# Kernel optimization log

Measured on AMD Instinct MI355X. Metric: run time of the kernel, lower is better.

Reference implementation:

```python
import math
import jax, jax.numpy as jnp
import numpy as np

B, T, C, H = 2, 2048, 1024, 16
MAX_SEQ = 2048


def _make_pe(max_seq: int, dim: int, base: float = 10000.0) -> np.ndarray:
    pe = np.zeros((max_seq, dim), dtype=np.float32)
    position = np.arange(max_seq, dtype=np.float32)[:, None]
    div_term = np.exp(np.arange(0, dim, 2, dtype=np.float32) * (-math.log(base) / dim))
    pe[:, 0::2] = np.sin(position * div_term)
    pe[:, 1::2] = np.cos(position * div_term)
    return pe


def setup_inputs() -> dict:
    key = jax.random.key(0)
    k1, k2, k3 = jax.random.split(key, 3)
    x = jax.random.normal(k1, (B, T, C), dtype=jnp.float32)
    # torch Linear default init scale ~ 1/sqrt(fan_in)
    w_qkv = jax.random.normal(k2, (3 * C, C), dtype=jnp.float32) / math.sqrt(C)
    w_proj = jax.random.normal(k3, (C, C), dtype=jnp.float32) / math.sqrt(C)
    pe = jnp.asarray(_make_pe(MAX_SEQ, C))
    return {"x": x, "w_qkv": w_qkv, "w_proj": w_proj, "pe": pe}


def reference(x, w_qkv, w_proj, pe):
    b, t, c = x.shape
    h = H
    d = c // h
    # RoPE module adds sinusoidal PE under torch.no_grad() -> stop_gradient
    xp = jax.lax.stop_gradient(x + pe[None, :t, :])
    qkv = xp @ w_qkv.T  # [b, t, 3c]
    q, k, v = jnp.split(qkv, 3, axis=-1)
    q = q.reshape(b, t, h, d).transpose(0, 2, 1, 3)  # bhtd
    k = k.reshape(b, t, h, d).transpose(0, 2, 1, 3)
    v = v.reshape(b, t, h, d).transpose(0, 2, 1, 3)
    att = jnp.einsum("bhqd,bhkd->bhqk", q, k) * (1.0 / math.sqrt(d))
    causal = jnp.tril(jnp.ones((t, t), dtype=bool))  # [t, t]
    att = jnp.where(causal[None, None], att, -jnp.inf)
    att = jax.nn.softmax(att, axis=-1)
    y = jnp.einsum("bhqk,bhkd->bhqd", att, v)
    y = y.transpose(0, 2, 1, 3).reshape(b, t, c)
    return y @ w_proj.T
```

## Files before the change

### kernel.cpp

```cpp
#include <hip/hip_runtime.h>
#include <cstdint>

typedef __bf16 bf16x8 __attribute__((ext_vector_type(8)));
typedef __bf16 bf16x4 __attribute__((ext_vector_type(4)));
typedef float  f32x4  __attribute__((ext_vector_type(4)));

static constexpr int kB = 2, kT = 2048, kC = 1024, kH = 16, kD = 64;
static constexpr int kK = 1024;

__device__ __forceinline__ uint16_t f2bf(float f) {
  uint32_t u = __builtin_bit_cast(uint32_t, f);
  u += 0x7FFFu + ((u >> 16) & 1u);
  return (uint16_t)(u >> 16);
}

__device__ __forceinline__ void gl_lds16(const void* g, void* l) {
  __builtin_amdgcn_global_load_lds((__attribute__((address_space(1))) void*)(void*)g,
                                   (__attribute__((address_space(3))) void*)l, 16, 0, 0);
}

__global__ __launch_bounds__(256) void prep_xpe(const float* __restrict__ x,
                                                const float* __restrict__ pe,
                                                uint16_t* __restrict__ xp) {
  const int i = blockIdx.x * 256 + threadIdx.x;
  const float4 xv = ((const float4*)x)[i];
  const int c4 = i & (kC / 4 - 1);
  const int t = (i / (kC / 4)) & (kT - 1);
  const float4 pv = ((const float4*)pe)[t * (kC / 4) + c4];
  ushort4 o;
  o.x = f2bf(xv.x + pv.x);
  o.y = f2bf(xv.y + pv.y);
  o.z = f2bf(xv.z + pv.z);
  o.w = f2bf(xv.w + pv.w);
  ((ushort4*)xp)[i] = o;
}

__global__ __launch_bounds__(256) void cast_w(const float* __restrict__ w,
                                              uint16_t* __restrict__ o) {
  const int i = blockIdx.x * 256 + threadIdx.x;
  const float4 v = ((const float4*)w)[i];
  ushort4 u;
  u.x = f2bf(v.x); u.y = f2bf(v.y); u.z = f2bf(v.z); u.w = f2bf(v.w);
  ((ushort4*)o)[i] = u;
}

template <int EPI>
__global__ __launch_bounds__(256) void gemm_bt(const uint16_t* __restrict__ A,
                                               const uint16_t* __restrict__ W,
                                               uint16_t* __restrict__ qb,
                                               uint16_t* __restrict__ kb,
                                               uint16_t* __restrict__ vT,
                                               float* __restrict__ out) {
  __shared__ __align__(1024) char lds[EPI == 0 ? 34816 : 32768];
  const int lane = threadIdx.x & 63;
  const int wid = threadIdx.x >> 6;
  const int l15 = lane & 15, l4 = lane >> 4;
  const int wm = wid >> 1, wn = wid & 1;
  const int orig = (int)(blockIdx.y * gridDim.x + blockIdx.x);
  const int xcd = orig & 7, j = orig >> 3;
  const int m0 = (xcd * 4 + (j & 3)) * 128;
  const int n0 = (j >> 2) * 128;

  f32x4 acc[4][4] = {};

  for (int k0 = 0; k0 < kK; k0 += 64) {
#pragma unroll
    for (int jj = 0; jj < 4; ++jj) {
      const int off = wid * 4096 + jj * 1024 + lane * 16;
      const int row = off >> 7;
      const int colb = (off & 127) ^ ((row & 7) << 4);
      gl_lds16((const char*)A + ((size_t)(m0 + row) * kK + k0) * 2 + colb,
               lds + wid * 4096 + jj * 1024);
      gl_lds16((const char*)W + ((size_t)(n0 + row) * kK + k0) * 2 + colb,
               lds + 16384 + wid * 4096 + jj * 1024);
    }
    __syncthreads();
#pragma unroll
    for (int ks = 0; ks < 2; ++ks) {
      bf16x8 af[4], bf_[4];
#pragma unroll
      for (int mt = 0; mt < 4; ++mt) {
        const int r = wm * 64 + mt * 16 + l15;
        const int cb = (l4 * 16 + ks * 64) ^ ((r & 7) << 4);
        af[mt] = *(const bf16x8*)(lds + r * 128 + cb);
      }
#pragma unroll
      for (int nt = 0; nt < 4; ++nt) {
        const int r = wn * 64 + nt * 16 + l15;
        const int cb = (l4 * 16 + ks * 64) ^ ((r & 7) << 4);
        bf_[nt] = *(const bf16x8*)(lds + 16384 + r * 128 + cb);
      }
#pragma unroll
      for (int mt = 0; mt < 4; ++mt)
#pragma unroll
        for (int nt = 0; nt < 4; ++nt)
          acc[mt][nt] = __builtin_amdgcn_mfma_f32_16x16x32_bf16(af[mt], bf_[nt],
                                                                acc[mt][nt], 0, 0, 0);
    }
    __syncthreads();
  }

  if constexpr (EPI == 0) {
    const int sec = n0 >> 10;
    if (sec < 2) {
#pragma unroll
      for (int mt = 0; mt < 4; ++mt)
#pragma unroll
        for (int nt = 0; nt < 4; ++nt)
#pragma unroll
          for (int r = 0; r < 4; ++r) {
            const int m = wm * 64 + mt * 16 + l4 * 4 + r;
            const int n = wn * 64 + nt * 16 + l15;
            *(uint16_t*)(lds + m * 272 + ((n * 2) ^ (((m >> 2) & 3) << 4))) =
                f2bf(acc[mt][nt][r]);
          }
    } else {
#pragma unroll
      for (int mt = 0; mt < 4; ++mt)
#pragma unroll
        for (int nt = 0; nt < 4; ++nt)
#pragma unroll
          for (int r = 0; r < 4; ++r) {
            const int m = wm * 64 + mt * 16 + l4 * 4 + r;
            const int n = wn * 64 + nt * 16 + l15;
            *(uint16_t*)(lds + n * 272 + m * 2) = f2bf(acc[mt][nt][r]);
          }
    }
    __syncthreads();
    const int tid = threadIdx.x;
    const int b = m0 >> 11, tbase = m0 & (kT - 1);
    if (sec < 2) {
      uint16_t* dst = (sec == 0) ? qb : kb;
#pragma unroll
      for (int i = 0; i < 8; ++i) {
        const int g = i * 256 + tid;
        const int ml = g >> 4;
        const int c8 = (g & 15) * 8;
        const bf16x8 v =
            *(const bf16x8*)(lds + ml * 272 + ((c8 * 2) ^ (((ml >> 2) & 3) << 4)));
        const int nn = (n0 & (kC - 1)) + c8;
        const int h = nn >> 6, d = nn & 63;
        *(bf16x8*)(dst + ((size_t)((b * kH + h) * kT + tbase + ml)) * kD + d) = v;
      }
    } else {
#pragma unroll
      for (int i = 0; i < 8; ++i) {
        const int g = i * 256 + tid;
        const int dl = g >> 4;
        const int m8 = (g & 15) * 8;
        const bf16x8 v = *(const bf16x8*)(lds + dl * 272 + m8 * 2);
        const int nn = (n0 & (kC - 1)) + dl;
        const int h = nn >> 6, d = nn & 63;
        *(bf16x8*)(vT + ((size_t)((b * kH + h) * kD + d)) * kT + tbase + m8) = v;
      }
    }
  } else {
#pragma unroll
    for (int mt = 0; mt < 4; ++mt)
#pragma unroll
      for (int nt = 0; nt < 4; ++nt)
#pragma unroll
        for (int r = 0; r < 4; ++r) {
          const int m = m0 + wm * 64 + mt * 16 + l4 * 4 + r;
          const int n = n0 + wn * 64 + nt * 16 + l15;
          out[(size_t)m * kC + n] = acc[mt][nt][r];
        }
  }
}

__global__ __launch_bounds__(256, 4) void attn(const uint16_t* __restrict__ qb,
                                               const uint16_t* __restrict__ kb,
                                               const uint16_t* __restrict__ vT,
                                               uint16_t* __restrict__ y) {
  __shared__ __align__(1024) char lds[40960];
  const int lane = threadIdx.x & 63;
  const int wid = threadIdx.x >> 6;
  const int l15 = lane & 15, l4 = lane >> 4;
  const int bh = blockIdx.x;
  const int qt = (int)(gridDim.y - 1) - (int)blockIdx.y;
  const int q0 = qt * 64 + wid * 16;
  const size_t base = (size_t)bh * kT * kD;
  const uint16_t* Q = qb + base;
  const uint16_t* Kp = kb + base;
  const uint16_t* Vt = vT + base;
  char* P = lds + 32768 + wid * 2048;
  const int xr = (l15 & 7) << 4;

  bf16x8 qf[2];
#pragma unroll
  for (int ks = 0; ks < 2; ++ks) {
    bf16x8 t = *(const bf16x8*)(Q + (size_t)(q0 + l15) * kD + ks * 32 + l4 * 8);
#pragma unroll
    for (int i = 0; i < 8; ++i) t[i] = (__bf16)((float)t[i] * 0.1803368801f);
    qf[ks] = t;
  }

  float m_ = -1e30f, l_ = 0.f;
  f32x4 o[4];
#pragma unroll
  for (int nt = 0; nt < 4; ++nt) o[nt] = (f32x4){0.f, 0.f, 0.f, 0.f};

  const int nkt = qt + 1;

  auto STAGE = [&](int bi, int k0) {
#pragma unroll
    for (int c = 0; c < 2; ++c) {
      const int call = wid * 2 + c;
      const int row = call * 8 + (lane >> 3);
      const int colb = (((lane & 7) ^ ((lane >> 3) & 7)) << 4);
      gl_lds16((const char*)Kp + ((size_t)(k0 + row) * kD) * 2 + colb,
               lds + bi * 8192 + call * 1024);
      gl_lds16((const char*)Vt + ((size_t)row * kT + k0) * 2 + colb,
               lds + 16384 + bi * 8192 + call * 1024);
    }
  };

  int cur = 0;
  STAGE(0, 0);
  for (int kt = 0; kt < nkt; ++kt) {
    const int k0 = kt * 64;
    const bool hasnext = (kt + 1 < nkt);
    if (hasnext) STAGE(cur ^ 1, k0 + 64);
    if (hasnext)
      asm volatile("s_waitcnt vmcnt(4)" ::: "memory");
    else
      asm volatile("s_waitcnt vmcnt(0)" ::: "memory");
    __builtin_amdgcn_s_barrier();
    asm volatile("" ::: "memory");

    const char* Kb = lds + cur * 8192;
    const char* Vb = lds + 16384 + cur * 8192;

    f32x4 s[4] = {};
    __builtin_amdgcn_s_setprio(1);
#pragma unroll
    for (int ks = 0; ks < 2; ++ks)
#pragma unroll
      for (int nt = 0; nt < 4; ++nt) {
        const bf16x8 kf =
            *(const bf16x8*)(Kb + (nt * 16 + l15) * 128 + ((ks * 64 + l4 * 16) ^ xr));
        s[nt] = __builtin_amdgcn_mfma_f32_16x16x32_bf16(kf, qf[ks], s[nt], 0, 0, 0);
      }
    __builtin_amdgcn_s_setprio(0);

    if (kt == nkt - 1) {
      const int qq = q0 + l15;
#pragma unroll
      for (int nt = 0; nt < 4; ++nt)
#pragma unroll
        for (int r = 0; r < 4; ++r)
          if (k0 + nt * 16 + l4 * 4 + r > qq) s[nt][r] = -1e30f;
    }

    float pm = s[0][0];
#pragma unroll
    for (int nt = 0; nt < 4; ++nt)
#pragma unroll
      for (int r = 0; r < 4; ++r) pm = fmaxf(pm, s[nt][r]);
    if (!__all(pm <= m_ + 11.0f)) {
      float rm = fmaxf(pm, __shfl_xor(pm, 16));
      rm = fmaxf(rm, __shfl_xor(rm, 32));
      const float newm = fmaxf(m_, rm);
      const float sc = exp2f(m_ - newm);
      m_ = newm;
      l_ *= sc;
#pragma unroll
      for (int nt = 0; nt < 4; ++nt)
#pragma unroll
        for (int r = 0; r < 4; ++r) o[nt][r] *= sc;
    }
    float ps = 0.f;
#pragma unroll
    for (int nt = 0; nt < 4; ++nt)
#pragma unroll
      for (int r = 0; r < 4; ++r) {
        const float p = exp2f(s[nt][r] - m_);
        s[nt][r] = p;
        ps += p;
      }
    l_ += ps;

#pragma unroll
    for (int nt = 0; nt < 4; ++nt) {
      bf16x4 pk;
#pragma unroll
      for (int r = 0; r < 4; ++r) pk[r] = (__bf16)s[nt][r];
      *(bf16x4*)(P + l15 * 128 + ((nt * 32 + l4 * 8) ^ xr)) = pk;
    }
    asm volatile("s_waitcnt lgkmcnt(0)" ::: "memory");
    __builtin_amdgcn_sched_barrier(0);

    bf16x8 pf[2];
#pragma unroll
    for (int ks = 0; ks < 2; ++ks)
      pf[ks] = *(const bf16x8*)(P + l15 * 128 + ((ks * 64 + l4 * 16) ^ xr));
    __builtin_amdgcn_s_setprio(1);
#pragma unroll
    for (int ks = 0; ks < 2; ++ks)
#pragma unroll
      for (int nt = 0; nt < 4; ++nt) {
        const bf16x8 vf =
            *(const bf16x8*)(Vb + (nt * 16 + l15) * 128 + ((ks * 64 + l4 * 16) ^ xr));
        o[nt] = __builtin_amdgcn_mfma_f32_16x16x32_bf16(vf, pf[ks], o[nt], 0, 0, 0);
      }
    __builtin_amdgcn_s_setprio(0);

    __builtin_amdgcn_s_barrier();
    asm volatile("" ::: "memory");
    cur ^= 1;
  }

  l_ += __shfl_xor(l_, 16);
  l_ += __shfl_xor(l_, 32);
  const float inv = 1.0f / l_;
  const int b = bh >> 4, h = bh & 15;
  const int q = q0 + l15;
#pragma unroll
  for (int nt = 0; nt < 4; ++nt) {
    bf16x4 yv;
#pragma unroll
    for (int r = 0; r < 4; ++r) yv[r] = (__bf16)(o[nt][r] * inv);
    *(bf16x4*)(y + ((size_t)(b * kT + q)) * kC + h * kD + nt * 16 + l4 * 4) = yv;
  }
}

extern "C" void kernel_launch(void* const* d_in, const int* in_sizes, int n_in,
                              void* d_out, int out_size, void* d_ws, size_t ws_size,
                              hipStream_t stream) {
  const float* x = (const float*)d_in[0];
  const float* wqkv = (const float*)d_in[1];
  const float* wproj = (const float*)d_in[2];
  const float* pe = (const float*)d_in[3];

  char* ws = (char*)d_ws;
  uint16_t* xp = (uint16_t*)(ws);
  uint16_t* wq = (uint16_t*)(ws + (size_t)(8u << 20));
  uint16_t* wp = (uint16_t*)(ws + (size_t)(14u << 20));
  uint16_t* qbuf = (uint16_t*)(ws + (size_t)(16u << 20));
  uint16_t* kbuf = (uint16_t*)(ws + (size_t)(24u << 20));
  uint16_t* vTb = (uint16_t*)(ws + (size_t)(32u << 20));

  prep_xpe<<<dim3(kB * kT * kC / 4 / 256), 256, 0, stream>>>(x, pe, xp);
  cast_w<<<dim3(3 * kC * kC / 4 / 256), 256, 0, stream>>>(wqkv, wq);
  cast_w<<<dim3(kC * kC / 4 / 256), 256, 0, stream>>>(wproj, wp);

  gemm_bt<0><<<dim3(32, 24), 256, 0, stream>>>(xp, wq, qbuf, kbuf, vTb, nullptr);

  attn<<<dim3(kB * kH, kT / 64), 256, 0, stream>>>(qbuf, kbuf, vTb, xp);

  gemm_bt<1><<<dim3(32, 8), 256, 0, stream>>>(xp, wp, nullptr, nullptr, nullptr,
                                              (float*)d_out);
}
```

Measured before the change: 119.9 us.

## Fuse prep kernels, retile QKV GEMM, and double attention query rows per warp

```diff
diff --git a/kernel.cpp b/kernel.cpp
--- a/kernel.cpp
+++ b/kernel.cpp
@@ -19,39 +19,171 @@
                                    (__attribute__((address_space(3))) void*)l, 16, 0, 0);
 }
 
-__global__ __launch_bounds__(256) void prep_xpe(const float* __restrict__ x,
+__global__ __launch_bounds__(256) void prep_all(const float* __restrict__ x,
                                                 const float* __restrict__ pe,
-                                                uint16_t* __restrict__ xp) {
+                                                const float* __restrict__ wqkv,
+                                                const float* __restrict__ wproj,
+                                                uint16_t* __restrict__ xp,
+                                                uint16_t* __restrict__ wq,
+                                                uint16_t* __restrict__ wp) {
+  constexpr int NX = kB * kT * kC / 4;
+  constexpr int NWQ = 3 * kC * kC / 4;
   const int i = blockIdx.x * 256 + threadIdx.x;
-  const float4 xv = ((const float4*)x)[i];
-  const int c4 = i & (kC / 4 - 1);
-  const int t = (i / (kC / 4)) & (kT - 1);
-  const float4 pv = ((const float4*)pe)[t * (kC / 4) + c4];
-  ushort4 o;
-  o.x = f2bf(xv.x + pv.x);
-  o.y = f2bf(xv.y + pv.y);
-  o.z = f2bf(xv.z + pv.z);
-  o.w = f2bf(xv.w + pv.w);
-  ((ushort4*)xp)[i] = o;
-}
-
-__global__ __launch_bounds__(256) void cast_w(const float* __restrict__ w,
-                                              uint16_t* __restrict__ o) {
-  const int i = blockIdx.x * 256 + threadIdx.x;
-  const float4 v = ((const float4*)w)[i];
-  ushort4 u;
-  u.x = f2bf(v.x); u.y = f2bf(v.y); u.z = f2bf(v.z); u.w = f2bf(v.w);
-  ((ushort4*)o)[i] = u;
-}
-
-template <int EPI>
-__global__ __launch_bounds__(256) void gemm_bt(const uint16_t* __restrict__ A,
-                                               const uint16_t* __restrict__ W,
-                                               uint16_t* __restrict__ qb,
-                                               uint16_t* __restrict__ kb,
-                                               uint16_t* __restrict__ vT,
-                                               float* __restrict__ out) {
-  __shared__ __align__(1024) char lds[EPI == 0 ? 34816 : 32768];
+  if (i < NX) {
+    const float4 xv = ((const float4*)x)[i];
+    const int c4 = i & (kC / 4 - 1);
+    const int t = (i / (kC / 4)) & (kT - 1);
+    const float4 pv = ((const float4*)pe)[t * (kC / 4) + c4];
+    ushort4 o;
+    o.x = f2bf(xv.x + pv.x);
+    o.y = f2bf(xv.y + pv.y);
+    o.z = f2bf(xv.z + pv.z);
+    o.w = f2bf(xv.w + pv.w);
+    ((ushort4*)xp)[i] = o;
+  } else if (i < NX + NWQ) {
+    const int j = i - NX;
+    const float4 v = ((const float4*)wqkv)[j];
+    ushort4 u;
+    u.x = f2bf(v.x); u.y = f2bf(v.y); u.z = f2bf(v.z); u.w = f2bf(v.w);
+    ((ushort4*)wq)[j] = u;
+  } else {
+    const int j = i - NX - NWQ;
+    const float4 v = ((const float4*)wproj)[j];
+    ushort4 u;
+    u.x = f2bf(v.x); u.y = f2bf(v.y); u.z = f2bf(v.z); u.w = f2bf(v.w);
+    ((ushort4*)wp)[j] = u;
+  }
+}
+
+__global__ __launch_bounds__(512, 2) void gemm_qkv(const uint16_t* __restrict__ A,
+                                                   const uint16_t* __restrict__ W,
+                                                   uint16_t* __restrict__ qb,
+                                                   uint16_t* __restrict__ kb,
+                                                   uint16_t* __restrict__ vT) {
+  __shared__ __align__(1024) char lds[114688];
+  const int tid = threadIdx.x;
+  const int lane = tid & 63;
+  const int l15 = lane & 15, l4 = lane >> 4;
+  const int wid = tid >> 6;
+  const int WM = wid >> 1, WN = wid & 1;
+  const int orig = (int)blockIdx.x;
+  const int xcd = orig & 7, j = orig >> 3;
+  const int m0 = (xcd * 2 + (j & 1)) * 256;
+  const int n0 = (j >> 1) * 192;
+
+  f32x4 acc[4][6] = {};
+
+  auto stageA = [&](int buf, int kt) {
+#pragma unroll
+    for (int c = 0; c < 4; ++c) {
+      const int off = (c * 512 + tid) * 16;
+      const int lr = off >> 7, cbl = off & 127;
+      gl_lds16((const char*)A + ((size_t)(m0 + lr) * kK + kt * 64) * 2 +
+                   (cbl ^ ((lr & 7) << 4)),
+               lds + buf * 32768 + off);
+    }
+  };
+  auto stageB = [&](int buf, int kt) {
+#pragma unroll
+    for (int c = 0; c < 3; ++c) {
+      const int off = (c * 512 + tid) * 16;
+      const int lr = off >> 7, cbl = off & 127;
+      gl_lds16((const char*)W + ((size_t)(n0 + lr) * kK + kt * 64) * 2 +
+                   (cbl ^ ((lr & 7) << 4)),
+               lds + 65536 + buf * 24576 + off);
+    }
+  };
+
+  bf16x8 af[2][4], bfr[2][3];
+  auto readA = [&](int buf) {
+#pragma unroll
+    for (int ks = 0; ks < 2; ++ks)
+#pragma unroll
+      for (int mt = 0; mt < 4; ++mt) {
+        const int r = WM * 64 + mt * 16 + l15;
+        af[ks][mt] = *(const bf16x8*)(lds + buf * 32768 + r * 128 +
+                                      ((ks * 64 + l4 * 16) ^ ((r & 7) << 4)));
+      }
+  };
+  auto readB = [&](int buf, int qc) {
+#pragma unroll
+    for (int ks = 0; ks < 2; ++ks)
+#pragma unroll
+      for (int ntl = 0; ntl < 3; ++ntl) {
+        const int r = WN * 96 + qc * 48 + ntl * 16 + l15;
+        bfr[ks][ntl] = *(const bf16x8*)(lds + 65536 + buf * 24576 + r * 128 +
+                                        ((ks * 64 + l4 * 16) ^ ((r & 7) << 4)));
+      }
+  };
+  auto mfma6 = [&](int qc) {
+    __builtin_amdgcn_s_setprio(1);
+#pragma unroll
+    for (int ks = 0; ks < 2; ++ks)
+#pragma unroll
+      for (int mt = 0; mt < 4; ++mt)
+#pragma unroll
+        for (int ntl = 0; ntl < 3; ++ntl)
+          acc[mt][qc * 3 + ntl] = __builtin_amdgcn_mfma_f32_16x16x32_bf16(
+              af[ks][mt], bfr[ks][ntl], acc[mt][qc * 3 + ntl], 0, 0, 0);
+    __builtin_amdgcn_s_setprio(0);
+  };
+
+  stageA(0, 0);
+  stageB(0, 0);
+
+  for (int i = 0; i < 8; ++i) {
+    int ktn = 2 * i + 2;
+    if (ktn > 15) ktn = 15;
+    stageA(1, 2 * i + 1);
+    asm volatile("s_waitcnt vmcnt(4)" ::: "memory");
+    __builtin_amdgcn_s_barrier();
+    asm volatile("" ::: "memory");
+    readA(0); readB(0, 0); mfma6(0);
+    stageB(1, 2 * i + 1);
+    readB(0, 1); mfma6(1);
+    asm volatile("" ::: "memory");
+    __builtin_amdgcn_s_barrier();
+    asm volatile("" ::: "memory");
+    stageA(0, ktn);
+    asm volatile("s_waitcnt vmcnt(4)" ::: "memory");
+    __builtin_amdgcn_s_barrier();
+    asm volatile("" ::: "memory");
+    readA(1); readB(1, 0); mfma6(0 + 0);
+    stageB(0, ktn);
+    readB(1, 1); mfma6(1);
+    asm volatile("" ::: "memory");
+    __builtin_amdgcn_s_barrier();
+    asm volatile("" ::: "memory");
+  }
+
+  const int b = m0 >> 11, tb = m0 & (kT - 1);
+#pragma unroll
+  for (int mt = 0; mt < 4; ++mt)
+#pragma unroll
+    for (int qc = 0; qc < 2; ++qc)
+#pragma unroll
+      for (int ntl = 0; ntl < 3; ++ntl)
+#pragma unroll
+        for (int r = 0; r < 4; ++r) {
+          const int m = WM * 64 + mt * 16 + l4 * 4 + r;
+          const int t = tb + m;
+          const int n = n0 + WN * 96 + qc * 48 + ntl * 16 + l15;
+          const int sec = n >> 10, nn = n & (kC - 1);
+          const int h = nn >> 6, d = nn & 63;
+          const uint16_t v = f2bf(acc[mt][qc * 3 + ntl][r]);
+          if (sec == 0)
+            qb[((size_t)((b * kH + h) * kT + t)) * kD + d] = v;
+          else if (sec == 1)
+            kb[((size_t)((b * kH + h) * kT + t)) * kD + d] = v;
+          else
+            vT[((size_t)((b * kH + h) * kD + d)) * kT + t] = v;
+        }
+}
+
+__global__ __launch_bounds__(256) void gemm_proj(const uint16_t* __restrict__ A,
+                                                 const uint16_t* __restrict__ W,
+                                                 float* __restrict__ out) {
+  __shared__ __align__(1024) char lds[32768];
   const int lane = threadIdx.x & 63;
   const int wid = threadIdx.x >> 6;
   const int l15 = lane & 15, l4 = lane >> 4;
@@ -100,107 +232,52 @@
     __syncthreads();
   }
 
-  if constexpr (EPI == 0) {
-    const int sec = n0 >> 10;
-    if (sec < 2) {
-#pragma unroll
-      for (int mt = 0; mt < 4; ++mt)
-#pragma unroll
-        for (int nt = 0; nt < 4; ++nt)
-#pragma unroll
-          for (int r = 0; r < 4; ++r) {
-            const int m = wm * 64 + mt * 16 + l4 * 4 + r;
-            const int n = wn * 64 + nt * 16 + l15;
-            *(uint16_t*)(lds + m * 272 + ((n * 2) ^ (((m >> 2) & 3) << 4))) =
-                f2bf(acc[mt][nt][r]);
-          }
-    } else {
-#pragma unroll
-      for (int mt = 0; mt < 4; ++mt)
-#pragma unroll
-        for (int nt = 0; nt < 4; ++nt)
-#pragma unroll
-          for (int r = 0; r < 4; ++r) {
-            const int m = wm * 64 + mt * 16 + l4 * 4 + r;
-            const int n = wn * 64 + nt * 16 + l15;
-            *(uint16_t*)(lds + n * 272 + m * 2) = f2bf(acc[mt][nt][r]);
-          }
-    }
-    __syncthreads();
-    const int tid = threadIdx.x;
-    const int b = m0 >> 11, tbase = m0 & (kT - 1);
-    if (sec < 2) {
-      uint16_t* dst = (sec == 0) ? qb : kb;
-#pragma unroll
-      for (int i = 0; i < 8; ++i) {
-        const int g = i * 256 + tid;
-        const int ml = g >> 4;
-        const int c8 = (g & 15) * 8;
-        const bf16x8 v =
-            *(const bf16x8*)(lds + ml * 272 + ((c8 * 2) ^ (((ml >> 2) & 3) << 4)));
-        const int nn = (n0 & (kC - 1)) + c8;
-        const int h = nn >> 6, d = nn & 63;
-        *(bf16x8*)(dst + ((size_t)((b * kH + h) * kT + tbase + ml)) * kD + d) = v;
-      }
-    } else {
-#pragma unroll
-      for (int i = 0; i < 8; ++i) {
-        const int g = i * 256 + tid;
-        const int dl = g >> 4;
-        const int m8 = (g & 15) * 8;
-        const bf16x8 v = *(const bf16x8*)(lds + dl * 272 + m8 * 2);
-        const int nn = (n0 & (kC - 1)) + dl;
-        const int h = nn >> 6, d = nn & 63;
-        *(bf16x8*)(vT + ((size_t)((b * kH + h) * kD + d)) * kT + tbase + m8) = v;
-      }
-    }
-  } else {
-#pragma unroll
-    for (int mt = 0; mt < 4; ++mt)
-#pragma unroll
-      for (int nt = 0; nt < 4; ++nt)
-#pragma unroll
-        for (int r = 0; r < 4; ++r) {
-          const int m = m0 + wm * 64 + mt * 16 + l4 * 4 + r;
-          const int n = n0 + wn * 64 + nt * 16 + l15;
-          out[(size_t)m * kC + n] = acc[mt][nt][r];
-        }
-  }
-}
-
-__global__ __launch_bounds__(256, 4) void attn(const uint16_t* __restrict__ qb,
+#pragma unroll
+  for (int mt = 0; mt < 4; ++mt)
+#pragma unroll
+    for (int nt = 0; nt < 4; ++nt)
+#pragma unroll
+      for (int r = 0; r < 4; ++r) {
+        const int m = m0 + wm * 64 + mt * 16 + l4 * 4 + r;
+        const int n = n0 + wn * 64 + nt * 16 + l15;
+        out[(size_t)m * kC + n] = acc[mt][nt][r];
+      }
+}
+
+__global__ __launch_bounds__(256, 3) void attn(const uint16_t* __restrict__ qb,
                                                const uint16_t* __restrict__ kb,
                                                const uint16_t* __restrict__ vT,
                                                uint16_t* __restrict__ y) {
-  __shared__ __align__(1024) char lds[40960];
+  __shared__ __align__(1024) char lds[49152];
   const int lane = threadIdx.x & 63;
   const int wid = threadIdx.x >> 6;
   const int l15 = lane & 15, l4 = lane >> 4;
   const int bh = blockIdx.x;
   const int qt = (int)(gridDim.y - 1) - (int)blockIdx.y;
-  const int q0 = qt * 64 + wid * 16;
+  const int q0w = qt * 128 + wid * 32;
   const size_t base = (size_t)bh * kT * kD;
   const uint16_t* Q = qb + base;
   const uint16_t* Kp = kb + base;
   const uint16_t* Vt = vT + base;
-  char* P = lds + 32768 + wid * 2048;
+  char* P = lds + 32768 + wid * 4096;
   const int xr = (l15 & 7) << 4;
 
-  bf16x8 qf[2];
-#pragma unroll
-  for (int ks = 0; ks < 2; ++ks) {
-    bf16x8 t = *(const bf16x8*)(Q + (size_t)(q0 + l15) * kD + ks * 32 + l4 * 8);
-#pragma unroll
-    for (int i = 0; i < 8; ++i) t[i] = (__bf16)((float)t[i] * 0.1803368801f);
-    qf[ks] = t;
-  }
-
-  float m_ = -1e30f, l_ = 0.f;
-  f32x4 o[4];
-#pragma unroll
-  for (int nt = 0; nt < 4; ++nt) o[nt] = (f32x4){0.f, 0.f, 0.f, 0.f};
-
-  const int nkt = qt + 1;
+  bf16x8 qf[2][2];
+#pragma unroll
+  for (int h = 0; h < 2; ++h)
+#pragma unroll
+    for (int ks = 0; ks < 2; ++ks) {
+      bf16x8 t = *(const bf16x8*)(Q + (size_t)(q0w + h * 16 + l15) * kD + ks * 32 + l4 * 8);
+#pragma unroll
+      for (int i = 0; i < 8; ++i) t[i] = (__bf16)((float)t[i] * 0.1803368801f);
+      qf[h][ks] = t;
+    }
+
+  float m_[2] = {0.f, 0.f}, l_[2] = {0.f, 0.f};
+  f32x4 o[2][4] = {};
+
+  const int nkt = 2 * qt + 2;
+  const int qwmax = q0w + 31;
 
   auto STAGE = [&](int bi, int k0) {
 #pragma unroll
@@ -228,99 +305,125 @@
     __builtin_amdgcn_s_barrier();
     asm volatile("" ::: "memory");
 
-    const char* Kb = lds + cur * 8192;
-    const char* Vb = lds + 16384 + cur * 8192;
-
-    f32x4 s[4] = {};
-    __builtin_amdgcn_s_setprio(1);
-#pragma unroll
-    for (int ks = 0; ks < 2; ++ks)
-#pragma unroll
-      for (int nt = 0; nt < 4; ++nt) {
-        const bf16x8 kf =
-            *(const bf16x8*)(Kb + (nt * 16 + l15) * 128 + ((ks * 64 + l4 * 16) ^ xr));
-        s[nt] = __builtin_amdgcn_mfma_f32_16x16x32_bf16(kf, qf[ks], s[nt], 0, 0, 0);
-      }
-    __builtin_amdgcn_s_setprio(0);
-
-    if (kt == nkt - 1) {
-      const int qq = q0 + l15;
-#pragma unroll
-      for (int nt = 0; nt < 4; ++nt)
-#pragma unroll
-        for (int r = 0; r < 4; ++r)
-          if (k0 + nt * 16 + l4 * 4 + r > qq) s[nt][r] = -1e30f;
-    }
-
-    float pm = s[0][0];
-#pragma unroll
-    for (int nt = 0; nt < 4; ++nt)
-#pragma unroll
-      for (int r = 0; r < 4; ++r) pm = fmaxf(pm, s[nt][r]);
-    if (!__all(pm <= m_ + 11.0f)) {
-      float rm = fmaxf(pm, __shfl_xor(pm, 16));
-      rm = fmaxf(rm, __shfl_xor(rm, 32));
-      const float newm = fmaxf(m_, rm);
-      const float sc = exp2f(m_ - newm);
-      m_ = newm;
-      l_ *= sc;
-#pragma unroll
-      for (int nt = 0; nt < 4; ++nt)
-#pragma unroll
-        for (int r = 0; r < 4; ++r) o[nt][r] *= sc;
-    }
-    float ps = 0.f;
-#pragma unroll
-    for (int nt = 0; nt < 4; ++nt)
-#pragma unroll
-      for (int r = 0; r < 4; ++r) {
-        const float p = exp2f(s[nt][r] - m_);
-        s[nt][r] = p;
-        ps += p;
-      }
-    l_ += ps;
-
-#pragma unroll
-    for (int nt = 0; nt < 4; ++nt) {
-      bf16x4 pk;
-#pragma unroll
-      for (int r = 0; r < 4; ++r) pk[r] = (__bf16)s[nt][r];
-      *(bf16x4*)(P + l15 * 128 + ((nt * 32 + l4 * 8) ^ xr)) = pk;
-    }
-    asm volatile("s_waitcnt lgkmcnt(0)" ::: "memory");
-    __builtin_amdgcn_sched_barrier(0);
-
-    bf16x8 pf[2];
-#pragma unroll
-    for (int ks = 0; ks < 2; ++ks)
-      pf[ks] = *(const bf16x8*)(P + l15 * 128 + ((ks * 64 + l4 * 16) ^ xr));
-    __builtin_amdgcn_s_setprio(1);
-#pragma unroll
-    for (int ks = 0; ks < 2; ++ks)
-#pragma unroll
-      for (int nt = 0; nt < 4; ++nt) {
-        const bf16x8 vf =
-            *(const bf16x8*)(Vb + (nt * 16 + l15) * 128 + ((ks * 64 + l4 * 16) ^ xr));
-        o[nt] = __builtin_amdgcn_mfma_f32_16x16x32_bf16(vf, pf[ks], o[nt], 0, 0, 0);
-      }
-    __builtin_amdgcn_s_setprio(0);
+    if (k0 <= qwmax) {
+      const char* Kb = lds + cur * 8192;
+      const char* Vb = lds + 16384 + cur * 8192;
+
+      f32x4 s[2][4];
+#pragma unroll
+      for (int h = 0; h < 2; ++h)
+#pragma unroll
+        for (int nt = 0; nt < 4; ++nt)
+          s[h][nt] = (f32x4){-m_[h], -m_[h], -m_[h], -m_[h]};
+      __builtin_amdgcn_s_setprio(1);
+#pragma unroll
+      for (int ks = 0; ks < 2; ++ks)
+#pragma unroll
+        for (int nt = 0; nt < 4; ++nt) {
+          const bf16x8 kf =
+              *(const bf16x8*)(Kb + (nt * 16 + l15) * 128 + ((ks * 64 + l4 * 16) ^ xr));
+          s[0][nt] = __builtin_amdgcn_mfma_f32_16x16x32_bf16(kf, qf[0][ks], s[0][nt], 0, 0, 0);
+          s[1][nt] = __builtin_amdgcn_mfma_f32_16x16x32_bf16(kf, qf[1][ks], s[1][nt], 0, 0, 0);
+        }
+      __builtin_amdgcn_s_setprio(0);
+
+#pragma unroll
+      for (int h = 0; h < 2; ++h) {
+        if (k0 + 63 > q0w + h * 16) {
+          const int qq = q0w + h * 16 + l15;
+#pragma unroll
+          for (int nt = 0; nt < 4; ++nt)
+#pragma unroll
+            for (int r = 0; r < 4; ++r)
+              if (k0 + nt * 16 + l4 * 4 + r > qq) s[h][nt][r] = -1e30f;
+        }
+        float pm = s[h][0][0];
+#pragma unroll
+        for (int nt = 0; nt < 4; ++nt)
+#pragma unroll
+          for (int r = 0; r < 4; ++r) pm = fmaxf(pm, s[h][nt][r]);
+        float ps = 0.f;
+        if (__all(pm <= 11.0f)) {
+#pragma unroll
+          for (int nt = 0; nt < 4; ++nt)
+#pragma unroll
+            for (int r = 0; r < 4; ++r) {
+              const float p = exp2f(s[h][nt][r]);
+              s[h][nt][r] = p;
+              ps += p;
+            }
+        } else {
+          float rm = fmaxf(pm, __shfl_xor(pm, 16));
+          rm = fmaxf(rm, __shfl_xor(rm, 32));
+          const float rmc = fmaxf(rm, 0.f);
+          const float sc = exp2f(-rmc);
+          m_[h] += rmc;
+          l_[h] *= sc;
+#pragma unroll
+          for (int nt = 0; nt < 4; ++nt)
+#pragma unroll
+            for (int r = 0; r < 4; ++r) o[h][nt][r] *= sc;
+#pragma unroll
+          for (int nt = 0; nt < 4; ++nt)
+#pragma unroll
+            for (int r = 0; r < 4; ++r) {
+              const float p = exp2f(s[h][nt][r] - rmc);
+              s[h][nt][r] = p;
+              ps += p;
+            }
+        }
+        l_[h] += ps;
+
+#pragma unroll
+        for (int nt = 0; nt < 4; ++nt) {
+          bf16x4 pk;
+#pragma unroll
+          for (int r = 0; r < 4; ++r) pk[r] = (__bf16)s[h][nt][r];
+          *(bf16x4*)(P + h * 2048 + l15 * 128 + ((nt * 32 + l4 * 8) ^ xr)) = pk;
+        }
+      }
+      asm volatile("s_waitcnt lgkmcnt(0)" ::: "memory");
+      __builtin_amdgcn_sched_barrier(0);
+
+      bf16x8 pf[2][2];
+#pragma unroll
+      for (int h = 0; h < 2; ++h)
+#pragma unroll
+        for (int ks = 0; ks < 2; ++ks)
+          pf[h][ks] =
+              *(const bf16x8*)(P + h * 2048 + l15 * 128 + ((ks * 64 + l4 * 16) ^ xr));
+      __builtin_amdgcn_s_setprio(1);
+#pragma unroll
+      for (int ks = 0; ks < 2; ++ks)
+#pragma unroll
+        for (int nt = 0; nt < 4; ++nt) {
+          const bf16x8 vf =
+              *(const bf16x8*)(Vb + (nt * 16 + l15) * 128 + ((ks * 64 + l4 * 16) ^ xr));
+          o[0][nt] = __builtin_amdgcn_mfma_f32_16x16x32_bf16(vf, pf[0][ks], o[0][nt], 0, 0, 0);
+          o[1][nt] = __builtin_amdgcn_mfma_f32_16x16x32_bf16(vf, pf[1][ks], o[1][nt], 0, 0, 0);
+        }
+      __builtin_amdgcn_s_setprio(0);
+    }
 
     __builtin_amdgcn_s_barrier();
     asm volatile("" ::: "memory");
     cur ^= 1;
   }
 
-  l_ += __shfl_xor(l_, 16);
-  l_ += __shfl_xor(l_, 32);
-  const float inv = 1.0f / l_;
-  const int b = bh >> 4, h = bh & 15;
-  const int q = q0 + l15;
-#pragma unroll
-  for (int nt = 0; nt < 4; ++nt) {
-    bf16x4 yv;
-#pragma unroll
-    for (int r = 0; r < 4; ++r) yv[r] = (__bf16)(o[nt][r] * inv);
-    *(bf16x4*)(y + ((size_t)(b * kT + q)) * kC + h * kD + nt * 16 + l4 * 4) = yv;
+  const int b = bh >> 4, h16 = bh & 15;
+#pragma unroll
+  for (int h = 0; h < 2; ++h) {
+    float lsum = l_[h] + __shfl_xor(l_[h], 16);
+    lsum += __shfl_xor(lsum, 32);
+    const float inv = 1.0f / lsum;
+    const int q = q0w + h * 16 + l15;
+#pragma unroll
+    for (int nt = 0; nt < 4; ++nt) {
+      bf16x4 yv;
+#pragma unroll
+      for (int r = 0; r < 4; ++r) yv[r] = (__bf16)(o[h][nt][r] * inv);
+      *(bf16x4*)(y + ((size_t)(b * kT + q)) * kC + h16 * kD + nt * 16 + l4 * 4) = yv;
+    }
   }
 }
 
@@ -340,14 +443,11 @@
   uint16_t* kbuf = (uint16_t*)(ws + (size_t)(24u << 20));
   uint16_t* vTb = (uint16_t*)(ws + (size_t)(32u << 20));
 
-  prep_xpe<<<dim3(kB * kT * kC / 4 / 256), 256, 0, stream>>>(x, pe, xp);
-  cast_w<<<dim3(3 * kC * kC / 4 / 256), 256, 0, stream>>>(wqkv, wq);
-  cast_w<<<dim3(kC * kC / 4 / 256), 256, 0, stream>>>(wproj, wp);
-
-  gemm_bt<0><<<dim3(32, 24), 256, 0, stream>>>(xp, wq, qbuf, kbuf, vTb, nullptr);
-
-  attn<<<dim3(kB * kH, kT / 64), 256, 0, stream>>>(qbuf, kbuf, vTb, xp);
-
-  gemm_bt<1><<<dim3(32, 8), 256, 0, stream>>>(xp, wp, nullptr, nullptr, nullptr,
-                                              (float*)d_out);
-}
+  prep_all<<<dim3(8192), 256, 0, stream>>>(x, pe, wqkv, wproj, xp, wq, wp);
+
+  gemm_qkv<<<dim3(256), 512, 0, stream>>>(xp, wq, qbuf, kbuf, vTb);
+
+  attn<<<dim3(kB * kH, kT / 128), 256, 0, stream>>>(qbuf, kbuf, vTb, xp);
+
+  gemm_proj<<<dim3(32, 8), 256, 0, stream>>>(xp, wp, (float*)d_out);
+}
```

Measured after the change: 130.6 us. 1.09x slower.
